# Kernel tuning notes

Measured on AMD Instinct MI355X. Metric: run time of the kernel, lower is better.

## Reference

```python
import jax, jax.numpy as jnp
import numpy as np

GROUP_SIZE = 8
OUT_FEATURES = 4096
IN_FEATURES = 4096
G = OUT_FEATURES * IN_FEATURES // GROUP_SIZE  # number of quant groups


def setup_inputs() -> dict:
    key = jax.random.key(0)
    k1, k2, k3, k4, k5 = jax.random.split(key, 5)
    x = jax.random.normal(k1, (2, 2048, IN_FEATURES), dtype=jnp.float32)
    # packed uint8 bytes, stored as int32 for harness dtype support (values 0..255)
    weight_packed = jax.random.randint(k2, (G, GROUP_SIZE // 2), 0, 256, dtype=jnp.int32)
    weight_scale = jax.random.uniform(k3, (G, 1), dtype=jnp.float32)
    weight_bias = jax.random.normal(k4, (G, 1), dtype=jnp.float32)
    bias = jax.random.normal(k5, (OUT_FEATURES,), dtype=jnp.float32)
    return {"x": x, "weight_packed": weight_packed, "weight_scale": weight_scale,
            "weight_bias": weight_bias, "bias": bias}


def dequantize_4bit(packed, scale, wbias):
    # packed: [G, gs//2] ints in [0,256); each byte holds two 4-bit values
    low = (packed & 15).astype(jnp.float32)          # even positions
    high = ((packed >> 4) & 15).astype(jnp.float32)  # odd positions
    # interleave: q[:, ::2] = low, q[:, 1::2] = high
    q = jnp.stack([low, high], axis=-1).reshape(packed.shape[0], -1)  # [G, gs]
    return q * scale + wbias  # per-group scale and bias, broadcast [G,1]->[G,gs]


def reference(x, weight_packed, weight_scale, weight_bias, bias):
    w = dequantize_4bit(weight_packed, weight_scale, weight_bias)
    w = w.reshape(OUT_FEATURES, IN_FEATURES)
    # F.linear: y = x @ w.T + bias
    return jnp.einsum('bsi,oi->bso', x, w) + bias
```

## Files before the change

### kernel.cpp

```cpp
#include <hip/hip_runtime.h>
#include <hip/hip_bf16.h>
#include <stdint.h>

#define M_DIM 4096
#define N_DIM 4096
#define K_DIM 4096
#define NGROUPS (N_DIM * K_DIM / 8)

typedef __attribute__((ext_vector_type(4))) float f32x4;
typedef __attribute__((ext_vector_type(8))) short bf16x8;
typedef __attribute__((ext_vector_type(4))) int   i32x4;

__device__ __forceinline__ ushort f2bf(float f) {
  union { float f; uint32_t u; } v; v.f = f;
  uint32_t r = v.u + 0x7FFFu + ((v.u >> 16) & 1u);
  return (ushort)(r >> 16);
}

__global__ void k_dequant_w(const int* __restrict__ wp, const float* __restrict__ wsc,
                            const float* __restrict__ wbs, ushort* __restrict__ W) {
  const int g = blockIdx.x * 256 + threadIdx.x;
  i32x4 p = *(const i32x4*)(wp + (size_t)g * 4);
  const float s = wsc[g];
  const float b = wbs[g];
  bf16x8 o;
#pragma unroll
  for (int j = 0; j < 4; ++j) {
    const float lo = (float)(p[j] & 15)        * s + b;
    const float hi = (float)((p[j] >> 4) & 15) * s + b;
    o[2 * j]     = (short)f2bf(lo);
    o[2 * j + 1] = (short)f2bf(hi);
  }
  *(bf16x8*)(W + (size_t)g * 8) = o;
}

__global__ void k_cvt_x(const float* __restrict__ x, ushort* __restrict__ X) {
  const int t = blockIdx.x * 256 + threadIdx.x;
  f32x4 a = *(const f32x4*)(x + (size_t)t * 8);
  f32x4 b = *(const f32x4*)(x + (size_t)t * 8 + 4);
  bf16x8 o;
#pragma unroll
  for (int j = 0; j < 4; ++j) {
    o[j]     = (short)f2bf(a[j]);
    o[4 + j] = (short)f2bf(b[j]);
  }
  *(bf16x8*)(X + (size_t)t * 8) = o;
}


#define GLD(src, dst) __builtin_amdgcn_global_load_lds(                        \
    (const __attribute__((address_space(1))) void*)(src),                      \
    (__attribute__((address_space(3))) void*)(dst), 16, 0, 0)

__global__ __launch_bounds__(512, 2) void k_gemm_8ph(
    const ushort* __restrict__ A, const ushort* __restrict__ B,
    const float* __restrict__ bias, float* __restrict__ C) {
  __shared__ ushort sA[2][256 * 64];
  __shared__ ushort sB[2][256 * 64];
  const int tid  = threadIdx.x;
  const int lane = tid & 63;
  const int wid  = tid >> 6;
  const int wr   = wid >> 2;
  const int wc   = wid & 3;
  const int bm = blockIdx.x >> 4;
  const int bn = blockIdx.x & 15;

  const ushort* Ab = A + (size_t)bm * 256 * K_DIM;
  const ushort* Bb = B + (size_t)bn * 256 * K_DIM;

  const int srow = tid >> 3;
  const int scc  = (tid & 7) ^ ((tid >> 3) & 7);
  const int dofs = (tid >> 6) * 64 * 8;

  const int l15   = lane & 15;
  const int kx    = (lane >> 4) * 8;
  const int xsw   = (lane & 7) << 3;
  const int kidx0 = (0 * 32 + kx) ^ xsw;
  const int kidx1 = (1 * 32 + kx) ^ xsw;
  const int abase = (wr * 128 + l15) * 64;
  const int bbase = (wc * 64 + l15) * 64;

  f32x4 acc[8][4] = {};

#define STAGE_A(buf, kko)                                                      \
  _Pragma("unroll") for (int j = 0; j < 4; ++j)                                \
      GLD(Ab + (size_t)(j * 64 + srow) * K_DIM + (kko) + scc * 8,              \
          &sA[buf][j * 4096 + dofs]);
#define STAGE_B(buf, kko)                                                      \
  _Pragma("unroll") for (int j = 0; j < 4; ++j)                                \
      GLD(Bb + (size_t)(j * 64 + srow) * K_DIM + (kko) + scc * 8,              \
          &sB[buf][j * 4096 + dofs]);

  STAGE_A(0, 0);
  STAGE_B(0, 0);
  __syncthreads();

  for (int t = 0; t < 64; ++t) {
    const int b  = t & 1;
    const int kk = t * 64;
    const ushort* sAb = sA[b];
    const ushort* sBb = sB[b];
    bf16x8 af[4][2], bf0[2][2], bf1[2][2];

#pragma unroll
    for (int m = 0; m < 4; ++m) {
      af[m][0] = *(const bf16x8*)(sAb + abase + m * 1024 + kidx0);
      af[m][1] = *(const bf16x8*)(sAb + abase + m * 1024 + kidx1);
    }
#pragma unroll
    for (int n = 0; n < 2; ++n) {
      bf0[n][0] = *(const bf16x8*)(sBb + bbase + n * 1024 + kidx0);
      bf0[n][1] = *(const bf16x8*)(sBb + bbase + n * 1024 + kidx1);
    }
    if (t < 63) { STAGE_A(b ^ 1, kk + 64); }
    __builtin_amdgcn_s_barrier();
    __builtin_amdgcn_s_setprio(1);
#pragma unroll
    for (int m = 0; m < 4; ++m)
#pragma unroll
      for (int n = 0; n < 2; ++n)
#pragma unroll
        for (int kc = 0; kc < 2; ++kc)
          acc[m][n] = __builtin_amdgcn_mfma_f32_16x16x32_bf16(
              af[m][kc], bf0[n][kc], acc[m][n], 0, 0, 0);
    __builtin_amdgcn_s_setprio(0);
    __builtin_amdgcn_s_barrier();

#pragma unroll
    for (int n = 0; n < 2; ++n) {
      bf1[n][0] = *(const bf16x8*)(sBb + bbase + (2 + n) * 1024 + kidx0);
      bf1[n][1] = *(const bf16x8*)(sBb + bbase + (2 + n) * 1024 + kidx1);
    }
    if (t < 63) { STAGE_B(b ^ 1, kk + 64); }
    __builtin_amdgcn_s_barrier();
    __builtin_amdgcn_s_setprio(1);
#pragma unroll
    for (int m = 0; m < 4; ++m)
#pragma unroll
      for (int n = 0; n < 2; ++n)
#pragma unroll
        for (int kc = 0; kc < 2; ++kc)
          acc[m][2 + n] = __builtin_amdgcn_mfma_f32_16x16x32_bf16(
              af[m][kc], bf1[n][kc], acc[m][2 + n], 0, 0, 0);
    __builtin_amdgcn_s_setprio(0);
    __builtin_amdgcn_s_barrier();

#pragma unroll
    for (int m = 0; m < 4; ++m) {
      af[m][0] = *(const bf16x8*)(sAb + abase + (4 + m) * 1024 + kidx0);
      af[m][1] = *(const bf16x8*)(sAb + abase + (4 + m) * 1024 + kidx1);
    }
    __builtin_amdgcn_s_barrier();
    __builtin_amdgcn_s_setprio(1);
#pragma unroll
    for (int m = 0; m < 4; ++m)
#pragma unroll
      for (int n = 0; n < 2; ++n)
#pragma unroll
        for (int kc = 0; kc < 2; ++kc)
          acc[4 + m][2 + n] = __builtin_amdgcn_mfma_f32_16x16x32_bf16(
              af[m][kc], bf1[n][kc], acc[4 + m][2 + n], 0, 0, 0);
    __builtin_amdgcn_s_setprio(0);
    __builtin_amdgcn_s_barrier();

    __builtin_amdgcn_s_setprio(1);
#pragma unroll
    for (int m = 0; m < 4; ++m)
#pragma unroll
      for (int n = 0; n < 2; ++n)
#pragma unroll
        for (int kc = 0; kc < 2; ++kc)
          acc[4 + m][n] = __builtin_amdgcn_mfma_f32_16x16x32_bf16(
              af[m][kc], bf0[n][kc], acc[4 + m][n], 0, 0, 0);
    __builtin_amdgcn_s_setprio(0);

    __syncthreads();
  }

  const int fr = lane & 15;
  const int fq = lane >> 4;
  const int growbase = bm * 256 + wr * 128;
  const int gcolbase = bn * 256 + wc * 64;
#pragma unroll
  for (int ni = 0; ni < 4; ++ni) {
    const int col = gcolbase + ni * 16 + fr;
    const float bv = bias[col];
#pragma unroll
    for (int mi = 0; mi < 8; ++mi) {
      float* cp = C + (size_t)(growbase + mi * 16 + fq * 4) * N_DIM + col;
#pragma unroll
      for (int r = 0; r < 4; ++r)
        cp[(size_t)r * N_DIM] = acc[mi][ni][r] + bv;
    }
  }
}

__global__ void k_fallback(const float* __restrict__ x, const int* __restrict__ wp,
                           const float* __restrict__ wsc, const float* __restrict__ wbs,
                           const float* __restrict__ bias, float* __restrict__ y) {
  const int m = blockIdx.x;
  const int n = blockIdx.y * 256 + threadIdx.x;
  const float* xr = x + (size_t)m * K_DIM;
  const int gbase = n * (K_DIM / 8);
  float acc = 0.f;
  for (int g = 0; g < K_DIM / 8; ++g) {
    i32x4 p = *(const i32x4*)(wp + (size_t)(gbase + g) * 4);
    const float s = wsc[gbase + g];
    const float b = wbs[gbase + g];
    const float* xk = xr + g * 8;
#pragma unroll
    for (int j = 0; j < 4; ++j) {
      acc += ((float)(p[j] & 15)        * s + b) * xk[2 * j];
      acc += ((float)((p[j] >> 4) & 15) * s + b) * xk[2 * j + 1];
    }
  }
  y[(size_t)m * N_DIM + n] = acc + bias[n];
}

extern "C" void kernel_launch(void* const* d_in, const int* in_sizes, int n_in,
                              void* d_out, int out_size, void* d_ws, size_t ws_size,
                              hipStream_t stream) {
  const float* x    = (const float*)d_in[0];
  const int*   wp   = (const int*)d_in[1];
  const float* wsc  = (const float*)d_in[2];
  const float* wbs  = (const float*)d_in[3];
  const float* bias = (const float*)d_in[4];
  float* y = (float*)d_out;

  const size_t wbytes = (size_t)N_DIM * K_DIM * sizeof(ushort);
  const size_t xbytes = (size_t)M_DIM * K_DIM * sizeof(ushort);

  if (ws_size >= wbytes + xbytes) {
    ushort* Wbf = (ushort*)d_ws;
    ushort* Xbf = (ushort*)((char*)d_ws + wbytes);
    k_dequant_w<<<NGROUPS / 256, 256, 0, stream>>>(wp, wsc, wbs, Wbf);
    k_cvt_x<<<(M_DIM * K_DIM / 8) / 256, 256, 0, stream>>>(x, Xbf);
    k_gemm_8ph<<<16 * 16, 512, 0, stream>>>(Xbf, Wbf, bias, y);
  } else {
    k_fallback<<<dim3(M_DIM, N_DIM / 256), 256, 0, stream>>>(x, wp, wsc, wbs, bias, y);
  }
}
```

Before: 297.4 us.

## Software-pipeline LDS fragment loads across iterations and drop end-of-loop syncthreads

Restructures the GEMM main loop so the first A/B fragments for the next k-tile are read from the other LDS buffer at the end of the current iteration, overlapping them with the last MFMA phase. Global-to-LDS staging is issued earlier in each phase, and the trailing __syncthreads is replaced by an explicit vmcnt wait plus barrier before the final compute phase. This removes one barrier per iteration and hides LDS read latency. The cost is more live fragment registers and tighter reliance on correct manual wait/barrier ordering.

```diff
diff --git a/kernel.cpp b/kernel.cpp
--- a/kernel.cpp
+++ b/kernel.cpp
@@ -95,74 +95,76 @@
   STAGE_B(0, 0);
   __syncthreads();
 
+  bf16x8 af0[4][2], af1[4][2], bfA[2][2], bfB[2][2];
+#pragma unroll
+  for (int m = 0; m < 4; ++m) {
+    af0[m][0] = *(const bf16x8*)(sA[0] + abase + m * 1024 + kidx0);
+    af0[m][1] = *(const bf16x8*)(sA[0] + abase + m * 1024 + kidx1);
+  }
+#pragma unroll
+  for (int n = 0; n < 2; ++n) {
+    bfA[n][0] = *(const bf16x8*)(sB[0] + bbase + n * 1024 + kidx0);
+    bfA[n][1] = *(const bf16x8*)(sB[0] + bbase + n * 1024 + kidx1);
+  }
+
   for (int t = 0; t < 64; ++t) {
     const int b  = t & 1;
     const int kk = t * 64;
     const ushort* sAb = sA[b];
     const ushort* sBb = sB[b];
-    bf16x8 af[4][2], bf0[2][2], bf1[2][2];
-
+    const ushort* sAn = sA[b ^ 1];
+    const ushort* sBn = sB[b ^ 1];
+
+    if (t < 63) { STAGE_A(b ^ 1, kk + 64); }
+#pragma unroll
+    for (int n = 0; n < 2; ++n) {
+      bfB[n][0] = *(const bf16x8*)(sBb + bbase + (2 + n) * 1024 + kidx0);
+      bfB[n][1] = *(const bf16x8*)(sBb + bbase + (2 + n) * 1024 + kidx1);
+    }
+    __builtin_amdgcn_s_setprio(1);
+#pragma unroll
+    for (int m = 0; m < 4; ++m)
+#pragma unroll
+      for (int n = 0; n < 2; ++n)
+#pragma unroll
+        for (int kc = 0; kc < 2; ++kc)
+          acc[m][n] = __builtin_amdgcn_mfma_f32_16x16x32_bf16(
+              af0[m][kc], bfA[n][kc], acc[m][n], 0, 0, 0);
+    __builtin_amdgcn_s_setprio(0);
+    __builtin_amdgcn_s_barrier();
+
+    if (t < 63) { STAGE_B(b ^ 1, kk + 64); }
 #pragma unroll
     for (int m = 0; m < 4; ++m) {
-      af[m][0] = *(const bf16x8*)(sAb + abase + m * 1024 + kidx0);
-      af[m][1] = *(const bf16x8*)(sAb + abase + m * 1024 + kidx1);
-    }
-#pragma unroll
-    for (int n = 0; n < 2; ++n) {
-      bf0[n][0] = *(const bf16x8*)(sBb + bbase + n * 1024 + kidx0);
-      bf0[n][1] = *(const bf16x8*)(sBb + bbase + n * 1024 + kidx1);
-    }
-    if (t < 63) { STAGE_A(b ^ 1, kk + 64); }
+      af1[m][0] = *(const bf16x8*)(sAb + abase + (4 + m) * 1024 + kidx0);
+      af1[m][1] = *(const bf16x8*)(sAb + abase + (4 + m) * 1024 + kidx1);
+    }
+    __builtin_amdgcn_s_setprio(1);
+#pragma unroll
+    for (int m = 0; m < 4; ++m)
+#pragma unroll
+      for (int n = 0; n < 2; ++n)
+#pragma unroll
+        for (int kc = 0; kc < 2; ++kc)
+          acc[m][2 + n] = __builtin_amdgcn_mfma_f32_16x16x32_bf16(
+              af0[m][kc], bfB[n][kc], acc[m][2 + n], 0, 0, 0);
+    __builtin_amdgcn_s_setprio(0);
     __builtin_amdgcn_s_barrier();
-    __builtin_amdgcn_s_setprio(1);
-#pragma unroll
-    for (int m = 0; m < 4; ++m)
-#pragma unroll
-      for (int n = 0; n < 2; ++n)
-#pragma unroll
-        for (int kc = 0; kc < 2; ++kc)
-          acc[m][n] = __builtin_amdgcn_mfma_f32_16x16x32_bf16(
-              af[m][kc], bf0[n][kc], acc[m][n], 0, 0, 0);
-    __builtin_amdgcn_s_setprio(0);
+
+    __builtin_amdgcn_s_setprio(1);
+#pragma unroll
+    for (int m = 0; m < 4; ++m)
+#pragma unroll
+      for (int n = 0; n < 2; ++n)
+#pragma unroll
+        for (int kc = 0; kc < 2; ++kc)
+          acc[4 + m][2 + n] = __builtin_amdgcn_mfma_f32_16x16x32_bf16(
+              af1[m][kc], bfB[n][kc], acc[4 + m][2 + n], 0, 0, 0);
+    __builtin_amdgcn_s_setprio(0);
+
+    if (t < 63) { asm volatile("s_waitcnt vmcnt(0)" ::: "memory"); }
     __builtin_amdgcn_s_barrier();
-
-#pragma unroll
-    for (int n = 0; n < 2; ++n) {
-      bf1[n][0] = *(const bf16x8*)(sBb + bbase + (2 + n) * 1024 + kidx0);
-      bf1[n][1] = *(const bf16x8*)(sBb + bbase + (2 + n) * 1024 + kidx1);
-    }
-    if (t < 63) { STAGE_B(b ^ 1, kk + 64); }
-    __builtin_amdgcn_s_barrier();
-    __builtin_amdgcn_s_setprio(1);
-#pragma unroll
-    for (int m = 0; m < 4; ++m)
-#pragma unroll
-      for (int n = 0; n < 2; ++n)
-#pragma unroll
-        for (int kc = 0; kc < 2; ++kc)
-          acc[m][2 + n] = __builtin_amdgcn_mfma_f32_16x16x32_bf16(
-              af[m][kc], bf1[n][kc], acc[m][2 + n], 0, 0, 0);
-    __builtin_amdgcn_s_setprio(0);
-    __builtin_amdgcn_s_barrier();
-
-#pragma unroll
-    for (int m = 0; m < 4; ++m) {
-      af[m][0] = *(const bf16x8*)(sAb + abase + (4 + m) * 1024 + kidx0);
-      af[m][1] = *(const bf16x8*)(sAb + abase + (4 + m) * 1024 + kidx1);
-    }
-    __builtin_amdgcn_s_barrier();
-    __builtin_amdgcn_s_setprio(1);
-#pragma unroll
-    for (int m = 0; m < 4; ++m)
-#pragma unroll
-      for (int n = 0; n < 2; ++n)
-#pragma unroll
-        for (int kc = 0; kc < 2; ++kc)
-          acc[4 + m][2 + n] = __builtin_amdgcn_mfma_f32_16x16x32_bf16(
-              af[m][kc], bf1[n][kc], acc[4 + m][2 + n], 0, 0, 0);
-    __builtin_amdgcn_s_setprio(0);
-    __builtin_amdgcn_s_barrier();
-
+    asm volatile("" ::: "memory");
     __builtin_amdgcn_s_setprio(1);
 #pragma unroll
     for (int m = 0; m < 4; ++m)
@@ -171,10 +173,20 @@
 #pragma unroll
         for (int kc = 0; kc < 2; ++kc)
           acc[4 + m][n] = __builtin_amdgcn_mfma_f32_16x16x32_bf16(
-              af[m][kc], bf0[n][kc], acc[4 + m][n], 0, 0, 0);
-    __builtin_amdgcn_s_setprio(0);
-
-    __syncthreads();
+              af1[m][kc], bfA[n][kc], acc[4 + m][n], 0, 0, 0);
+    __builtin_amdgcn_s_setprio(0);
+    if (t < 63) {
+#pragma unroll
+      for (int m = 0; m < 4; ++m) {
+        af0[m][0] = *(const bf16x8*)(sAn + abase + m * 1024 + kidx0);
+        af0[m][1] = *(const bf16x8*)(sAn + abase + m * 1024 + kidx1);
+      }
+#pragma unroll
+      for (int n = 0; n < 2; ++n) {
+        bfA[n][0] = *(const bf16x8*)(sBn + bbase + n * 1024 + kidx0);
+        bfA[n][1] = *(const bf16x8*)(sBn + bbase + n * 1024 + kidx1);
+      }
+    }
   }
 
   const int fr = lane & 15;
```

New measurement: 301.0 us. Within noise of the previous version (+1.2%).
